# Optimization experiments

Measured on AMD Instinct MI355X. Metric: run time of the kernel, lower is better.

The kernel has to match this reference:

```python
import jax, jax.numpy as jnp
import numpy as np

BN_EPS = 1e-5

def _bn(x, gamma, beta):
    # BatchNorm1d in training mode: batch mean, biased variance
    m = jnp.mean(x, axis=0)
    v = jnp.var(x, axis=0)
    return (x - m) * jax.lax.rsqrt(v + BN_EPS) * gamma + beta

def setup_inputs() -> dict:
    key = jax.random.key(0)
    ks = jax.random.split(key, 12)
    N, E, D, ED = 50000, 600000, 128, 16
    s = lambda k, sh: jax.random.normal(k, sh, dtype=jnp.float32) * 0.05
    return {
        'h': jax.random.normal(ks[0], (N, D), dtype=jnp.float32),
        'edge_index': jax.random.randint(ks[1], (2, E), 0, N, dtype=jnp.int64),
        'edge_attr': jax.random.normal(ks[2], (E, ED), dtype=jnp.float32),
        'ee_w1': s(ks[3], (ED, D)), 'ee_b1': jnp.zeros((D,), jnp.float32),
        'ee_g1': jnp.ones((D,), jnp.float32), 'ee_bb1': jnp.zeros((D,), jnp.float32),
        'ee_w2': s(ks[4], (D, D)), 'ee_b2': jnp.zeros((D,), jnp.float32),
        'mlp_w1': s(ks[5], (D, D)), 'mlp_b1': jnp.zeros((D,), jnp.float32),
        'mlp_g1': jnp.ones((D,), jnp.float32), 'mlp_bb1': jnp.zeros((D,), jnp.float32),
        'mlp_w2': s(ks[6], (D, D)), 'mlp_b2': jnp.zeros((D,), jnp.float32),
        'mlp_g2': jnp.ones((D,), jnp.float32), 'mlp_bb2': jnp.zeros((D,), jnp.float32),
    }

def reference(h, edge_index, edge_attr, ee_w1, ee_b1, ee_g1, ee_bb1, ee_w2, ee_b2,
              mlp_w1, mlp_b1, mlp_g1, mlp_bb1, mlp_w2, mlp_b2, mlp_g2, mlp_bb2):
    N = h.shape[0]
    src, dst = edge_index[0], edge_index[1]
    # edge_encoder: Linear -> BN -> ReLU -> Linear
    e = jax.nn.relu(_bn(edge_attr @ ee_w1 + ee_b1, ee_g1, ee_bb1)) @ ee_w2 + ee_b2  # [E, D]
    # scatter-add edge embeddings to destination nodes
    agg_edge = jax.ops.segment_sum(e, dst, num_segments=N)  # [N, D]
    h = h + agg_edge
    # GINConv (eps=0): mlp(h + sum_{j->i} h_j)
    neigh = jax.ops.segment_sum(h[src], dst, num_segments=N)  # [N, D]
    z = h + neigh
    z = jax.nn.relu(_bn(z @ mlp_w1 + mlp_b1, mlp_g1, mlp_bb1))
    z = jax.nn.relu(_bn(z @ mlp_w2 + mlp_b2, mlp_g2, mlp_bb2))
    return z
```

## Files before the change

kernel.cpp:

```cpp
#include <hip/hip_runtime.h>
#include <hip/hip_bf16.h>

#define DD 128
#define EDIM 16

typedef short v8s __attribute__((ext_vector_type(8)));
typedef float v4f __attribute__((ext_vector_type(4)));

__device__ __forceinline__ float ldf(const void* p, int i, int bf){
  return bf ? __bfloat162float(((const __hip_bfloat16*)p)[i])
            : ((const float*)p)[i];
}
__device__ __forceinline__ float bfu_lo(unsigned u){
  unsigned b = (u & 0xffffu) << 16; float f; __builtin_memcpy(&f,&b,4); return f;
}
__device__ __forceinline__ float bfu_hi(unsigned u){
  unsigned b = u & 0xffff0000u; float f; __builtin_memcpy(&f,&b,4); return f;
}
__device__ __forceinline__ unsigned short f2bf(float f){
  unsigned u; __builtin_memcpy(&u,&f,4);
  unsigned r = (u + 0x7fffu + ((u>>16)&1u)) >> 16;
  return (unsigned short)r;
}
__device__ __forceinline__ unsigned packbf(float a, float b){
  return (unsigned)f2bf(a) | ((unsigned)f2bf(b) << 16);
}

__device__ __forceinline__ void load_attr_row(const void* __restrict__ attr,
                                              int e, int bf, float* a){
  if (bf){
    const uint4* ap = reinterpret_cast<const uint4*>(
        (const __hip_bfloat16*)attr + (size_t)e*EDIM);
    uint4 u0 = ap[0], u1 = ap[1];
    a[0]=bfu_lo(u0.x);  a[1]=bfu_hi(u0.x);  a[2]=bfu_lo(u0.y);  a[3]=bfu_hi(u0.y);
    a[4]=bfu_lo(u0.z);  a[5]=bfu_hi(u0.z);  a[6]=bfu_lo(u0.w);  a[7]=bfu_hi(u0.w);
    a[8]=bfu_lo(u1.x);  a[9]=bfu_hi(u1.x);  a[10]=bfu_lo(u1.y); a[11]=bfu_hi(u1.y);
    a[12]=bfu_lo(u1.z); a[13]=bfu_hi(u1.z); a[14]=bfu_lo(u1.w); a[15]=bfu_hi(u1.w);
  } else {
    const float4* ap = reinterpret_cast<const float4*>(
        (const float*)attr + (size_t)e*EDIM);
    float4 v0=ap[0], v1=ap[1], v2=ap[2], v3=ap[3];
    a[0]=v0.x; a[1]=v0.y; a[2]=v0.z; a[3]=v0.w;
    a[4]=v1.x; a[5]=v1.y; a[6]=v1.z; a[7]=v1.w;
    a[8]=v2.x; a[9]=v2.y; a[10]=v2.z; a[11]=v2.w;
    a[12]=v3.x;a[13]=v3.y;a[14]=v3.z; a[15]=v3.w;
  }
}

__global__ void k_detect(const void* g1, const int* ei, int E, int* flags){
  __shared__ int nz;
  if (threadIdx.x==0) nz = 0;
  __syncthreads();
  long long total = 2LL*E;
  long long stride = (total/1024) & ~1LL;
  if (stride < 2) stride = 2;
  long long idx = (long long)threadIdx.x*stride + 1;
  if (idx < total && ei[idx] != 0) atomicAdd(&nz, 1);
  __syncthreads();
  if (threadIdx.x==0){
    unsigned w = *(const unsigned*)g1;
    flags[0] = (w == 0x3F803F80u) ? 1 : 0;
    flags[1] = (nz == 0) ? 1 : 0;
  }
}

__global__ void k_transB(const void* w0, const void* w1, const void* w2,
                         const void* we1, const int* __restrict__ flags,
                         short* __restrict__ Bt){
  const int bf = flags[0];
  for (int idx = blockIdx.x*blockDim.x + threadIdx.x; idx < 3*16384 + 2048;
       idx += gridDim.x*blockDim.x){
    if (idx < 3*16384){
      int m = idx >> 14, r = idx & 16383;
      int nn = r >> 7, k = r & 127;
      const void* w = (m==0) ? w0 : ((m==1) ? w1 : w2);
      Bt[idx] = (short)f2bf(ldf(w, k*DD + nn, bf));
    } else {
      int r = idx - 3*16384;
      int nn = r >> 4, k = r & 15;
      Bt[idx] = (short)f2bf(ldf(we1, k*DD + nn, bf));
    }
  }
}

__global__ __launch_bounds__(256) void k_attr_moments(
    const void* __restrict__ attr, int E, const int* __restrict__ flags,
    float* __restrict__ Ssum, float* __restrict__ csum)
{
  const int bf = flags[0];
  float acc[136];
  #pragma unroll
  for (int i=0;i<136;++i) acc[i]=0.f;
  float cs[EDIM];
  #pragma unroll
  for (int i=0;i<EDIM;++i) cs[i]=0.f;

  for (int e = blockIdx.x*blockDim.x + threadIdx.x; e < E;
       e += gridDim.x*blockDim.x){
    float a[EDIM];
    load_attr_row(attr, e, bf, a);
    int idx = 0;
    #pragma unroll
    for (int p=0;p<EDIM;++p){
      cs[p] += a[p];
      #pragma unroll
      for (int q=p;q<EDIM;++q){
        acc[idx] = fmaf(a[p], a[q], acc[idx]);
        ++idx;
      }
    }
  }
  #pragma unroll
  for (int i=0;i<136;++i){
    float v = acc[i];
    #pragma unroll
    for (int off=32; off>0; off>>=1) v += __shfl_down(v, off, 64);
    acc[i] = v;
  }
  #pragma unroll
  for (int i=0;i<EDIM;++i){
    float v = cs[i];
    #pragma unroll
    for (int off=32; off>0; off>>=1) v += __shfl_down(v, off, 64);
    cs[i] = v;
  }
  __shared__ float red[4][152];
  const int wave = threadIdx.x >> 6, lane = threadIdx.x & 63;
  if (lane==0){
    for (int i=0;i<136;++i) red[wave][i] = acc[i];
    for (int i=0;i<EDIM;++i) red[wave][136+i] = cs[i];
  }
  __syncthreads();
  const int t = threadIdx.x;
  if (t < 152){
    float s = red[0][t]+red[1][t]+red[2][t]+red[3][t];
    if (t < 136) atomicAdd(&Ssum[t], s);
    else         atomicAdd(&csum[t-136], s);
  }
}

__global__ void k_edge_bn(const void* __restrict__ w1, const void* __restrict__ g,
                          const void* __restrict__ bb,
                          const float* __restrict__ Ssum, const float* __restrict__ csum,
                          float Einv, const int* __restrict__ flags,
                          float* __restrict__ sc, float* __restrict__ sh){
  const int j = threadIdx.x;
  const int bf = flags[0];
  float w[EDIM];
  #pragma unroll
  for (int p=0;p<EDIM;++p) w[p] = ldf(w1, p*DD + j, bf);
  float mu0 = 0.f;
  #pragma unroll
  for (int p=0;p<EDIM;++p) mu0 += csum[p]*Einv*w[p];
  float s2 = 0.f;
  #pragma unroll
  for (int p=0;p<EDIM;++p){
    float acc = 0.f;
    #pragma unroll
    for (int q=0;q<EDIM;++q){
      int tp = p < q ? p : q, tq = p < q ? q : p;
      int idx = 16*tp - (tp*(tp+1))/2 + tq;
      acc += Ssum[idx]*w[q];
    }
    s2 += w[p]*acc;
  }
  float var = s2*Einv - mu0*mu0;
  float scv = ldf(g, j, bf) * rsqrtf(var + 1e-5f);
  sc[j] = scv;
  sh[j] = ldf(bb, j, bf) - mu0*scv;
}

__global__ void k_hist(const int* __restrict__ ei, int E,
                       const int* __restrict__ flags, int* __restrict__ deg){
  const int i64 = flags[1];
  const int2* ei2 = (const int2*)ei;
  for (int e = blockIdx.x*blockDim.x + threadIdx.x; e < E;
       e += gridDim.x*blockDim.x){
    int d = i64 ? ei2[E + e].x : ei[E + e];
    atomicAdd(&deg[d], 1);
  }
}

__global__ void k_scan_partial(const int* __restrict__ deg, int n,
                               int* __restrict__ bsum){
  __shared__ int red[256];
  const int t = threadIdx.x;
  const int base = blockIdx.x*1024;
  int s = 0;
  for (int i = t; i < 1024; i += 256){
    int g = base + i;
    s += (g < n) ? deg[g] : 0;
  }
  red[t] = s; __syncthreads();
  for (int off=128; off>0; off>>=1){
    if (t < off) red[t] += red[t+off];
    __syncthreads();
  }
  if (t==0) bsum[blockIdx.x] = red[0];
}

__global__ void k_scan_tops(int* __restrict__ bsum, int nb, int* __restrict__ total){
  __shared__ int buf[256];
  const int t = threadIdx.x;
  int v = (t < nb) ? bsum[t] : 0;
  buf[t] = v; __syncthreads();
  for (int off=1; off<256; off<<=1){
    int x = (t>=off) ? buf[t-off] : 0;
    __syncthreads();
    buf[t] += x; __syncthreads();
  }
  if (t < nb) bsum[t] = buf[t] - v;
  if (t == 255) *total = buf[255];
}

__global__ void k_scan_final(const int* __restrict__ deg, int n,
                             const int* __restrict__ bsum, const int* __restrict__ total,
                             int* __restrict__ offsets, int* __restrict__ cursor){
  __shared__ int red[256];
  const int t = threadIdx.x;
  const int base = blockIdx.x*1024 + t*4;
  int v[4]; int s = 0;
  #pragma unroll
  for (int k=0;k<4;++k){
    int g = base + k;
    v[k] = (g < n) ? deg[g] : 0;
    s += v[k];
  }
  red[t] = s; __syncthreads();
  for (int off=1; off<256; off<<=1){
    int x = (t>=off) ? red[t-off] : 0;
    __syncthreads();
    red[t] += x; __syncthreads();
  }
  int ex = bsum[blockIdx.x] + red[t] - s;
  #pragma unroll
  for (int k=0;k<4;++k){
    int g = base + k;
    if (g < n){ offsets[g] = ex; cursor[g] = ex; }
    ex += v[k];
  }
  if (blockIdx.x==0 && t==0) offsets[n] = *total;
}

__global__ void k_scatter(const int* __restrict__ ei, const void* __restrict__ attr,
                          int E, const int* __restrict__ flags,
                          int* __restrict__ cursor,
                          int* __restrict__ esrc, unsigned* __restrict__ attrpH){
  const int i64 = flags[1];
  const int bf = flags[0];
  const int2* ei2 = (const int2*)ei;
  for (int e = blockIdx.x*blockDim.x + threadIdx.x; e < E;
       e += gridDim.x*blockDim.x){
    int d = i64 ? ei2[E + e].x : ei[E + e];
    int s = i64 ? ei2[e].x     : ei[e];
    int pp = atomicAdd(&cursor[d], 1);
    esrc[pp] = s;
    float a[EDIM];
    load_attr_row(attr, e, bf, a);
    uint4* dst = reinterpret_cast<uint4*>(attrpH + (size_t)pp*8);
    uint4 o0, o1;
    o0.x = packbf(a[0],a[1]);   o0.y = packbf(a[2],a[3]);
    o0.z = packbf(a[4],a[5]);   o0.w = packbf(a[6],a[7]);
    o1.x = packbf(a[8],a[9]);   o1.y = packbf(a[10],a[11]);
    o1.z = packbf(a[12],a[13]); o1.w = packbf(a[14],a[15]);
    dst[0] = o0; dst[1] = o1;
  }
}

__global__ __launch_bounds__(256) void k_edgemm(
    const short* __restrict__ attrpH, const short* __restrict__ w1t,
    const float* __restrict__ sc, const float* __restrict__ sh,
    int E, __hip_bfloat16* __restrict__ X)
{
  const int t = threadIdx.x;
  const int wv = t >> 6, lane = t & 63, l15 = lane & 15, quad = lane >> 4;
  const int S0 = blockIdx.x*64 + wv*16;
  v8s a = (v8s){0,0,0,0,0,0,0,0};
  if (quad < 2){
    int slot = S0 + l15;
    if (slot < E)
      a = *reinterpret_cast<const v8s*>(&attrpH[(size_t)slot*EDIM + quad*8]);
  }
  v4f acc[8];
  #pragma unroll
  for (int cg=0;cg<8;++cg) acc[cg] = (v4f){0.f,0.f,0.f,0.f};
  #pragma unroll
  for (int cg=0;cg<8;++cg){
    v8s b = (v8s){0,0,0,0,0,0,0,0};
    if (quad < 2)
      b = *reinterpret_cast<const v8s*>(&w1t[(cg*16+l15)*EDIM + quad*8]);
    acc[cg] = __builtin_amdgcn_mfma_f32_16x16x32_bf16(a, b, acc[cg], 0,0,0);
  }
  float scv[8], shv[8];
  #pragma unroll
  for (int cg=0;cg<8;++cg){ scv[cg]=sc[cg*16+l15]; shv[cg]=sh[cg*16+l15]; }
  #pragma unroll
  for (int reg=0;reg<4;++reg){
    int slot = S0 + quad*4 + reg;
    if (slot < E){
      #pragma unroll
      for (int cg=0;cg<8;++cg){
        float x = fmaxf(fmaf(acc[cg][reg], scv[cg], shv[cg]), 0.f);
        X[(size_t)slot*DD + cg*16 + l15] = __float2bfloat16(x);
      }
    }
  }
}

__global__ __launch_bounds__(256) void k_psum(
    const uint4* __restrict__ X16, const int* __restrict__ offsets,
    int n, uint4* __restrict__ PaggH16)
{
  const int wv = threadIdx.x >> 6, lane = threadIdx.x & 63;
  const int g = lane >> 4, c16 = lane & 15;
  for (int i = blockIdx.x*4 + wv; i < n; i += gridDim.x*4){
    const int beg = offsets[i], end = offsets[i+1];
    float a0=0.f,a1=0.f,a2=0.f,a3=0.f,a4=0.f,a5=0.f,a6=0.f,a7=0.f;
    for (int c0 = beg; c0 < end; c0 += 4){
      int r = c0 + g;
      if (r < end){
        uint4 u = X16[(size_t)r*16 + c16];
        a0 += bfu_lo(u.x); a1 += bfu_hi(u.x);
        a2 += bfu_lo(u.y); a3 += bfu_hi(u.y);
        a4 += bfu_lo(u.z); a5 += bfu_hi(u.z);
        a6 += bfu_lo(u.w); a7 += bfu_hi(u.w);
      }
    }
    a0 += __shfl_xor(a0,16,64); a1 += __shfl_xor(a1,16,64);
    a2 += __shfl_xor(a2,16,64); a3 += __shfl_xor(a3,16,64);
    a4 += __shfl_xor(a4,16,64); a5 += __shfl_xor(a5,16,64);
    a6 += __shfl_xor(a6,16,64); a7 += __shfl_xor(a7,16,64);
    a0 += __shfl_xor(a0,32,64); a1 += __shfl_xor(a1,32,64);
    a2 += __shfl_xor(a2,32,64); a3 += __shfl_xor(a3,32,64);
    a4 += __shfl_xor(a4,32,64); a5 += __shfl_xor(a5,32,64);
    a6 += __shfl_xor(a6,32,64); a7 += __shfl_xor(a7,32,64);
    if (lane < 16){
      uint4 o;
      o.x = packbf(a0,a1); o.y = packbf(a2,a3);
      o.z = packbf(a4,a5); o.w = packbf(a6,a7);
      PaggH16[(size_t)i*16 + lane] = o;
    }
  }
}

__global__ __launch_bounds__(256) void k_gather_z(
    const uint4* __restrict__ hnew16, const int* __restrict__ offsets,
    const int* __restrict__ esrc, int n, uint4* __restrict__ zH16)
{
  const int wv = threadIdx.x >> 6, lane = threadIdx.x & 63;
  const int g = lane >> 4, c16 = lane & 15;
  for (int i = blockIdx.x*4 + wv; i < n; i += gridDim.x*4){
    const int beg = offsets[i], end = offsets[i+1];
    float a0=0.f,a1=0.f,a2=0.f,a3=0.f,a4=0.f,a5=0.f,a6=0.f,a7=0.f;
    int c0 = beg;
    for (; c0 + 8 <= end; c0 += 8){
      int s1 = esrc[c0 + g];
      int s2 = esrc[c0 + 4 + g];
      uint4 u = hnew16[(size_t)s1*16 + c16];
      uint4 v = hnew16[(size_t)s2*16 + c16];
      a0 += bfu_lo(u.x)+bfu_lo(v.x); a1 += bfu_hi(u.x)+bfu_hi(v.x);
      a2 += bfu_lo(u.y)+bfu_lo(v.y); a3 += bfu_hi(u.y)+bfu_hi(v.y);
      a4 += bfu_lo(u.z)+bfu_lo(v.z); a5 += bfu_hi(u.z)+bfu_hi(v.z);
      a6 += bfu_lo(u.w)+bfu_lo(v.w); a7 += bfu_hi(u.w)+bfu_hi(v.w);
    }
    for (; c0 < end; c0 += 4){
      int r = c0 + g;
      if (r < end){
        uint4 u = hnew16[(size_t)esrc[r]*16 + c16];
        a0 += bfu_lo(u.x); a1 += bfu_hi(u.x);
        a2 += bfu_lo(u.y); a3 += bfu_hi(u.y);
        a4 += bfu_lo(u.z); a5 += bfu_hi(u.z);
        a6 += bfu_lo(u.w); a7 += bfu_hi(u.w);
      }
    }
    a0 += __shfl_xor(a0,16,64); a1 += __shfl_xor(a1,16,64);
    a2 += __shfl_xor(a2,16,64); a3 += __shfl_xor(a3,16,64);
    a4 += __shfl_xor(a4,16,64); a5 += __shfl_xor(a5,16,64);
    a6 += __shfl_xor(a6,16,64); a7 += __shfl_xor(a7,16,64);
    a0 += __shfl_xor(a0,32,64); a1 += __shfl_xor(a1,32,64);
    a2 += __shfl_xor(a2,32,64); a3 += __shfl_xor(a3,32,64);
    a4 += __shfl_xor(a4,32,64); a5 += __shfl_xor(a5,32,64);
    a6 += __shfl_xor(a6,32,64); a7 += __shfl_xor(a7,32,64);
    if (lane < 16){
      uint4 m = hnew16[(size_t)i*16 + lane];
      uint4 o;
      o.x = packbf(a0+bfu_lo(m.x), a1+bfu_hi(m.x));
      o.y = packbf(a2+bfu_lo(m.y), a3+bfu_hi(m.y));
      o.z = packbf(a4+bfu_lo(m.z), a5+bfu_hi(m.z));
      o.w = packbf(a6+bfu_lo(m.w), a7+bfu_hi(m.w));
      zH16[(size_t)i*16 + lane] = o;
    }
  }
}

__global__ __launch_bounds__(256) void k_gemm_mfma(
    const short* __restrict__ A, const short* __restrict__ Bt,
    const void* __restrict__ bias,
    const float* __restrict__ psc, const float* __restrict__ psh,
    const int* __restrict__ deg, const void* __restrict__ H,
    const int* __restrict__ flags, int n,
    __hip_bfloat16* __restrict__ out, float* __restrict__ stats, int mode)
{
  __shared__ float sb[256];
  const int t = threadIdx.x;
  const int bfi = flags[0];
  sb[t] = 0.f;
  __syncthreads();
  const int wv = t >> 6, lane = t & 63, l15 = lane & 15, quad = lane >> 4;
  const int R0 = blockIdx.x*64 + wv*16;

  v8s a[4];
  {
    const int arow = R0 + l15;
    const bool ok = (arow < n);
    #pragma unroll
    for (int ks=0;ks<4;++ks){
      const int k0 = ks*32 + quad*8;
      uint4 u = {0u,0u,0u,0u};
      if (ok) u = *reinterpret_cast<const uint4*>(&A[(size_t)arow*DD + k0]);
      if (psc){
        float f[8];
        f[0]=bfu_lo(u.x); f[1]=bfu_hi(u.x); f[2]=bfu_lo(u.y); f[3]=bfu_hi(u.y);
        f[4]=bfu_lo(u.z); f[5]=bfu_hi(u.z); f[6]=bfu_lo(u.w); f[7]=bfu_hi(u.w);
        v8s av;
        #pragma unroll
        for (int j=0;j<8;++j)
          av[j] = (short)f2bf(fmaxf(fmaf(f[j], psc[k0+j], psh[k0+j]), 0.f));
        a[ks] = av;
      } else {
        a[ks] = *reinterpret_cast<v8s*>(&u);
      }
    }
  }

  v4f acc[8];
  #pragma unroll
  for (int cg=0;cg<8;++cg) acc[cg] = (v4f){0.f,0.f,0.f,0.f};
  #pragma unroll
  for (int ks=0;ks<4;++ks){
    #pragma unroll
    for (int cg=0;cg<8;++cg){
      v8s b = *reinterpret_cast<const v8s*>(
                &Bt[(cg*16+l15)*DD + ks*32 + quad*8]);
      acc[cg] = __builtin_amdgcn_mfma_f32_16x16x32_bf16(a[ks], b, acc[cg], 0,0,0);
    }
  }

  float bc[8];
  #pragma unroll
  for (int cg=0;cg<8;++cg) bc[cg] = ldf(bias, cg*16 + l15, bfi);
  float ss[8], sq[8];
  #pragma unroll
  for (int cg=0;cg<8;++cg){ ss[cg]=0.f; sq[cg]=0.f; }

  #pragma unroll
  for (int reg=0;reg<4;++reg){
    const int row = R0 + quad*4 + reg;
    if (row < n){
      float degf = (mode==1) ? (float)deg[row] : 0.f;
      #pragma unroll
      for (int cg=0;cg<8;++cg){
        const int col = cg*16 + l15;
        float x = acc[cg][reg];
        if (mode==1) x = fmaf(degf, bc[cg], x) + ldf(H, (size_t)row*DD + col, bfi);
        else         x += bc[cg];
        out[(size_t)row*DD + col] = __float2bfloat16(x);
        ss[cg] += x; sq[cg] += x*x;
      }
    }
  }

  if (stats){
    #pragma unroll
    for (int cg=0;cg<8;++cg){
      float s = ss[cg], q = sq[cg];
      s += __shfl_xor(s, 16, 64); s += __shfl_xor(s, 32, 64);
      q += __shfl_xor(q, 16, 64); q += __shfl_xor(q, 32, 64);
      if (quad == 0){
        atomicAdd(&sb[cg*16 + l15], s);
        atomicAdd(&sb[128 + cg*16 + l15], q);
      }
    }
    __syncthreads();
    atomicAdd(&stats[t], sb[t]);
  }
}

__global__ void k_bn_params(const float* __restrict__ stats, const void* __restrict__ g,
                            const void* __restrict__ bb, const int* __restrict__ flags,
                            float inv_n, float* __restrict__ sc, float* __restrict__ sh){
  const int j = threadIdx.x;
  const int bf = flags[0];
  float mean = stats[j]*inv_n;
  float var  = stats[DD+j]*inv_n - mean*mean;
  float s = ldf(g, j, bf) * rsqrtf(var + 1e-5f);
  sc[j] = s;
  sh[j] = ldf(bb, j, bf) - mean*s;
}

__global__ void k_final(const unsigned* __restrict__ yH,
                        const float* __restrict__ sc, const float* __restrict__ sh,
                        int n, const int* __restrict__ flags, void* __restrict__ out){
  const int bf = flags[0];
  const int nw = n*64;
  for (int i = blockIdx.x*blockDim.x + threadIdx.x; i < nw;
       i += gridDim.x*blockDim.x){
    const int j0 = (i & 63)*2;
    unsigned u = yH[i];
    float v0 = fmaxf(fmaf(bfu_lo(u), sc[j0],   sh[j0]),   0.f);
    float v1 = fmaxf(fmaf(bfu_hi(u), sc[j0+1], sh[j0+1]), 0.f);
    if (bf){
      ((unsigned*)out)[i] = packbf(v0, v1);
    } else {
      *reinterpret_cast<float2*>((float*)out + 2*(size_t)i) = make_float2(v0, v1);
    }
  }
}

extern "C" void kernel_launch(void* const* d_in, const int* in_sizes, int n_in,
                              void* d_out, int out_size, void* d_ws, size_t ws_size,
                              hipStream_t stream)
{
  const void* h       = d_in[0];
  const int*  ei      = (const int*)d_in[1];
  const void* attr    = d_in[2];
  const void* ee_w1   = d_in[3];
  const void* ee_g1   = d_in[5];
  const void* ee_bb1  = d_in[6];
  const void* ee_w2   = d_in[7];
  const void* ee_b2   = d_in[8];
  const void* mlp_w1  = d_in[9];
  const void* mlp_b1  = d_in[10];
  const void* mlp_g1  = d_in[11];
  const void* mlp_bb1 = d_in[12];
  const void* mlp_w2  = d_in[13];
  const void* mlp_b2  = d_in[14];
  const void* mlp_g2  = d_in[15];
  const void* mlp_bb2 = d_in[16];

  const int N = in_sizes[0] / DD;
  const int E = in_sizes[1] / 2;
  const int nb = (N + 1023) / 1024;

  char* p = (char*)d_ws;
  auto alloc = [&](size_t bytes)->char*{
    char* r = p;
    p += (bytes + 255) & ~size_t(255);
    return r;
  };
  int* flags = (int*)alloc(8);
  char* zbase = p;
  int*   deg    = (int*)  zbase;
  float* csum   = (float*)(zbase + (size_t)N*4);
  float* Ssum   = (float*)(zbase + (size_t)N*4 + 64);
  float* stats1 = (float*)(zbase + (size_t)N*4 + 64 + 576);
  float* stats2 = (float*)(zbase + (size_t)N*4 + 64 + 576 + 1024);
  size_t zlen   = (size_t)N*4 + 64 + 576 + 1024 + 1024;
  p += (zlen + 255) & ~size_t(255);
  int*   bsum    = (int*)  alloc(256*4);
  int*   total   = (int*)  alloc(64);
  int*   offsets = (int*)  alloc((size_t)(N+1)*4);
  int*   cursor  = (int*)  alloc((size_t)N*4);
  int*   esrc    = (int*)  alloc((size_t)E*4);
  unsigned* attrpH = (unsigned*)alloc((size_t)E*EDIM*2);
  short* Bt      = (short*)alloc((size_t)(3*DD*DD + DD*EDIM)*2);
  short* w1t     = Bt + 3*DD*DD;
  float* ebn_sc  = (float*)alloc(512);
  float* ebn_sh  = (float*)alloc(512);
  float* sc1     = (float*)alloc(512);
  float* sh1     = (float*)alloc(512);
  float* sc2     = (float*)alloc(512);
  float* sh2     = (float*)alloc(512);
  short* PaggH   = (short*)alloc((size_t)N*DD*2);
  char*  Xreg    = alloc((size_t)E*DD*2);
  __hip_bfloat16* X = (__hip_bfloat16*)Xreg;
  short* hnewH = (short*)Xreg;
  short* zH    = (short*)(Xreg + (size_t)N*DD*2);
  short* y1H   = (short*)(Xreg + (size_t)N*DD*4);
  short* y2H   = (short*)(Xreg + (size_t)N*DD*6);
  (void)ws_size; (void)n_in; (void)out_size;

  const int g64  = (N + 63) / 64;
  const int e64  = (E + 63) / 64;
  const int gseg = (N + 15) / 16;

  hipMemsetAsync(zbase, 0, zlen, stream);
  k_detect<<<1, 1024, 0, stream>>>(ee_g1, ei, E, flags);
  k_transB<<<208, 256, 0, stream>>>(ee_w2, mlp_w1, mlp_w2, ee_w1, flags, Bt);
  k_attr_moments<<<512, 256, 0, stream>>>(attr, E, flags, Ssum, csum);
  k_edge_bn<<<1, 128, 0, stream>>>(ee_w1, ee_g1, ee_bb1, Ssum, csum,
                                   1.0f/(float)E, flags, ebn_sc, ebn_sh);
  k_hist<<<1024, 256, 0, stream>>>(ei, E, flags, deg);
  k_scan_partial<<<nb, 256, 0, stream>>>(deg, N, bsum);
  k_scan_tops<<<1, 256, 0, stream>>>(bsum, nb, total);
  k_scan_final<<<nb, 256, 0, stream>>>(deg, N, bsum, total, offsets, cursor);
  k_scatter<<<1024, 256, 0, stream>>>(ei, attr, E, flags, cursor, esrc, attrpH);

  k_edgemm<<<e64, 256, 0, stream>>>((const short*)attrpH, w1t, ebn_sc, ebn_sh,
                                    E, X);
  k_psum<<<gseg, 256, 0, stream>>>((const uint4*)X, offsets, N, (uint4*)PaggH);

  k_gemm_mfma<<<g64, 256, 0, stream>>>(PaggH, Bt, ee_b2, nullptr, nullptr,
                                       deg, h, flags, N,
                                       (__hip_bfloat16*)hnewH, nullptr, 1);
  k_gather_z<<<gseg, 256, 0, stream>>>((const uint4*)hnewH, offsets, esrc, N,
                                       (uint4*)zH);
  k_gemm_mfma<<<g64, 256, 0, stream>>>(zH, Bt + 16384, mlp_b1, nullptr, nullptr,
                                       nullptr, nullptr, flags, N,
                                       (__hip_bfloat16*)y1H, stats1, 0);
  k_bn_params<<<1, 128, 0, stream>>>(stats1, mlp_g1, mlp_bb1, flags,
                                     1.0f/(float)N, sc1, sh1);
  k_gemm_mfma<<<g64, 256, 0, stream>>>(y1H, Bt + 32768, mlp_b2, sc1, sh1,
                                       nullptr, nullptr, flags, N,
                                       (__hip_bfloat16*)y2H, stats2, 0);
  k_bn_params<<<1, 128, 0, stream>>>(stats2, mlp_g2, mlp_bb2, flags,
                                     1.0f/(float)N, sc2, sh2);

  k_final<<<2048, 256, 0, stream>>>((const unsigned*)y2H, sc2, sh2,
                                    N, flags, d_out);
}
```

Baseline: 472.7 us.

## Fuse edge encoder GEMM with segmented atomic aggregation; MFMA attribute moments

The edge-encoder first layer is now fused with the per-destination reduction. Each wave computes 16 dst-sorted edges and does segmented reductions, then atomically adds partial sums into an fp32 node buffer. This removes the E x 128 bf16 intermediate write and its re-read in the old psum kernel, at the cost of a zeroed N x 128 fp32 buffer, an extra snode array, and float atomics. The attribute second-moment kernel now builds a full 16x16 Gram matrix with one MFMA per 32-edge chunk instead of 136 per-thread scalar FMAs, and the downstream GEMM gains an fp32 input path.

```diff
diff --git a/kernel.cpp b/kernel.cpp
--- a/kernel.cpp
+++ b/kernel.cpp
@@ -85,57 +85,68 @@
 
 __global__ __launch_bounds__(256) void k_attr_moments(
     const void* __restrict__ attr, int E, const int* __restrict__ flags,
-    float* __restrict__ Ssum, float* __restrict__ csum)
+    float* __restrict__ Ssum , float* __restrict__ csum )
 {
+  __shared__ short Ws[4*512];
+  __shared__ float sred[4][256];
+  __shared__ float credu[4][16];
+  const int t = threadIdx.x;
+  const int wv = t >> 6, lane = t & 63, l15 = lane & 15, quad = lane >> 4;
   const int bf = flags[0];
-  float acc[136];
-  #pragma unroll
-  for (int i=0;i<136;++i) acc[i]=0.f;
-  float cs[EDIM];
-  #pragma unroll
-  for (int i=0;i<EDIM;++i) cs[i]=0.f;
-
-  for (int e = blockIdx.x*blockDim.x + threadIdx.x; e < E;
-       e += gridDim.x*blockDim.x){
-    float a[EDIM];
-    load_attr_row(attr, e, bf, a);
-    int idx = 0;
-    #pragma unroll
-    for (int p=0;p<EDIM;++p){
-      cs[p] += a[p];
-      #pragma unroll
-      for (int q=p;q<EDIM;++q){
-        acc[idx] = fmaf(a[p], a[q], acc[idx]);
-        ++idx;
-      }
-    }
-  }
-  #pragma unroll
-  for (int i=0;i<136;++i){
-    float v = acc[i];
-    #pragma unroll
-    for (int off=32; off>0; off>>=1) v += __shfl_down(v, off, 64);
-    acc[i] = v;
-  }
-  #pragma unroll
-  for (int i=0;i<EDIM;++i){
-    float v = cs[i];
-    #pragma unroll
-    for (int off=32; off>0; off>>=1) v += __shfl_down(v, off, 64);
-    cs[i] = v;
-  }
-  __shared__ float red[4][152];
-  const int wave = threadIdx.x >> 6, lane = threadIdx.x & 63;
-  if (lane==0){
-    for (int i=0;i<136;++i) red[wave][i] = acc[i];
-    for (int i=0;i<EDIM;++i) red[wave][136+i] = cs[i];
+  const int el = lane >> 1, half = lane & 1;
+  short* W = &Ws[wv*512];
+
+  v4f acc = (v4f){0.f,0.f,0.f,0.f};
+  float cs[8];
+  #pragma unroll
+  for (int j=0;j<8;++j) cs[j]=0.f;
+
+  const int nchunks = (E + 31) >> 5;
+  for (int c = blockIdx.x*4 + wv; c < nchunks; c += gridDim.x*4){
+    const int e = c*32 + el;
+    const bool ok = (e < E);
+    float f[8];
+    if (bf){
+      uint4 u = {0u,0u,0u,0u};
+      if (ok) u = reinterpret_cast<const uint4*>(attr)[(size_t)e*2 + half];
+      f[0]=bfu_lo(u.x); f[1]=bfu_hi(u.x); f[2]=bfu_lo(u.y); f[3]=bfu_hi(u.y);
+      f[4]=bfu_lo(u.z); f[5]=bfu_hi(u.z); f[6]=bfu_lo(u.w); f[7]=bfu_hi(u.w);
+    } else {
+      float4 v0 = {0,0,0,0}, v1 = {0,0,0,0};
+      if (ok){
+        const float4* ap = reinterpret_cast<const float4*>(attr) +
+                           (size_t)e*4 + half*2;
+        v0 = ap[0]; v1 = ap[1];
+      }
+      f[0]=v0.x; f[1]=v0.y; f[2]=v0.z; f[3]=v0.w;
+      f[4]=v1.x; f[5]=v1.y; f[6]=v1.z; f[7]=v1.w;
+    }
+    #pragma unroll
+    for (int j=0;j<8;++j){
+      cs[j] += f[j];
+      W[(half*8 + j)*32 + el] = (short)f2bf(f[j]);
+    }
+    v8s a = *reinterpret_cast<const v8s*>(&W[l15*32 + quad*8]);
+    acc = __builtin_amdgcn_mfma_f32_16x16x32_bf16(a, a, acc, 0,0,0);
+  }
+
+  #pragma unroll
+  for (int r=0;r<4;++r) sred[wv][(quad*4 + r)*16 + l15] = acc[r];
+  #pragma unroll
+  for (int j=0;j<8;++j){
+    #pragma unroll
+    for (int off=2; off<64; off<<=1) cs[j] += __shfl_xor(cs[j], off, 64);
+  }
+  if (lane < 2){
+    #pragma unroll
+    for (int j=0;j<8;++j) credu[wv][lane*8 + j] = cs[j];
   }
   __syncthreads();
-  const int t = threadIdx.x;
-  if (t < 152){
-    float s = red[0][t]+red[1][t]+red[2][t]+red[3][t];
-    if (t < 136) atomicAdd(&Ssum[t], s);
-    else         atomicAdd(&csum[t-136], s);
+  float s = sred[0][t]+sred[1][t]+sred[2][t]+sred[3][t];
+  atomicAdd(&Ssum[t], s);
+  if (t < 16){
+    float s2 = credu[0][t]+credu[1][t]+credu[2][t]+credu[3][t];
+    atomicAdd(&csum[t], s2);
   }
 }
 
@@ -157,11 +168,7 @@
   for (int p=0;p<EDIM;++p){
     float acc = 0.f;
     #pragma unroll
-    for (int q=0;q<EDIM;++q){
-      int tp = p < q ? p : q, tq = p < q ? q : p;
-      int idx = 16*tp - (tp*(tp+1))/2 + tq;
-      acc += Ssum[idx]*w[q];
-    }
+    for (int q=0;q<EDIM;++q) acc += Ssum[p*16 + q]*w[q];
     s2 += w[p]*acc;
   }
   float var = s2*Einv - mu0*mu0;
@@ -244,8 +251,8 @@
 
 __global__ void k_scatter(const int* __restrict__ ei, const void* __restrict__ attr,
                           int E, const int* __restrict__ flags,
-                          int* __restrict__ cursor,
-                          int* __restrict__ esrc, unsigned* __restrict__ attrpH){
+                          int* __restrict__ cursor, int* __restrict__ esrc,
+                          int* __restrict__ snode, unsigned* __restrict__ attrpH){
   const int i64 = flags[1];
   const int bf = flags[0];
   const int2* ei2 = (const int2*)ei;
@@ -255,6 +262,7 @@
     int s = i64 ? ei2[e].x     : ei[e];
     int pp = atomicAdd(&cursor[d], 1);
     esrc[pp] = s;
+    snode[pp] = d;
     float a[EDIM];
     load_attr_row(attr, e, bf, a);
     uint4* dst = reinterpret_cast<uint4*>(attrpH + (size_t)pp*8);
@@ -267,79 +275,68 @@
   }
 }
 
-__global__ __launch_bounds__(256) void k_edgemm(
+__global__ __launch_bounds__(256) void k_edgeagg(
     const short* __restrict__ attrpH, const short* __restrict__ w1t,
     const float* __restrict__ sc, const float* __restrict__ sh,
-    int E, __hip_bfloat16* __restrict__ X)
+    const int* __restrict__ offsets, const int* __restrict__ snode,
+    int n, int E, float* __restrict__ Pagg)
 {
   const int t = threadIdx.x;
   const int wv = t >> 6, lane = t & 63, l15 = lane & 15, quad = lane >> 4;
-  const int S0 = blockIdx.x*64 + wv*16;
+  const int W0 = blockIdx.x*64 + wv*16;
+  if (W0 >= E) return;
+
   v8s a = (v8s){0,0,0,0,0,0,0,0};
   if (quad < 2){
-    int slot = S0 + l15;
+    int slot = W0 + l15;
     if (slot < E)
       a = *reinterpret_cast<const v8s*>(&attrpH[(size_t)slot*EDIM + quad*8]);
   }
-  v4f acc[8];
-  #pragma unroll
-  for (int cg=0;cg<8;++cg) acc[cg] = (v4f){0.f,0.f,0.f,0.f};
+  float val[8][4];
   #pragma unroll
   for (int cg=0;cg<8;++cg){
     v8s b = (v8s){0,0,0,0,0,0,0,0};
     if (quad < 2)
       b = *reinterpret_cast<const v8s*>(&w1t[(cg*16+l15)*EDIM + quad*8]);
-    acc[cg] = __builtin_amdgcn_mfma_f32_16x16x32_bf16(a, b, acc[cg], 0,0,0);
-  }
-  float scv[8], shv[8];
-  #pragma unroll
-  for (int cg=0;cg<8;++cg){ scv[cg]=sc[cg*16+l15]; shv[cg]=sh[cg*16+l15]; }
-  #pragma unroll
-  for (int reg=0;reg<4;++reg){
-    int slot = S0 + quad*4 + reg;
-    if (slot < E){
+    v4f acc = (v4f){0.f,0.f,0.f,0.f};
+    acc = __builtin_amdgcn_mfma_f32_16x16x32_bf16(a, b, acc, 0,0,0);
+    const float scv = sc[cg*16+l15], shv = sh[cg*16+l15];
+    #pragma unroll
+    for (int reg=0;reg<4;++reg)
+      val[cg][reg] = fmaxf(fmaf(acc[reg], scv, shv), 0.f);
+  }
+
+  int i = snode[W0];
+  const int Wend = (W0 + 16 < E) ? (W0 + 16) : E;
+  int segb = W0;
+  while (segb < Wend && i < n){
+    int oe = offsets[i+1];
+    int sege = (oe < Wend) ? oe : Wend;
+    if (sege > segb){
+      float part[8];
+      #pragma unroll
+      for (int cg=0;cg<8;++cg) part[cg] = 0.f;
+      #pragma unroll
+      for (int reg=0;reg<4;++reg){
+        int s = W0 + quad*4 + reg;
+        if (s >= segb && s < sege){
+          #pragma unroll
+          for (int cg=0;cg<8;++cg) part[cg] += val[cg][reg];
+        }
+      }
       #pragma unroll
       for (int cg=0;cg<8;++cg){
-        float x = fmaxf(fmaf(acc[cg][reg], scv[cg], shv[cg]), 0.f);
-        X[(size_t)slot*DD + cg*16 + l15] = __float2bfloat16(x);
-      }
-    }
-  }
-}
-
-__global__ __launch_bounds__(256) void k_psum(
-    const uint4* __restrict__ X16, const int* __restrict__ offsets,
-    int n, uint4* __restrict__ PaggH16)
-{
-  const int wv = threadIdx.x >> 6, lane = threadIdx.x & 63;
-  const int g = lane >> 4, c16 = lane & 15;
-  for (int i = blockIdx.x*4 + wv; i < n; i += gridDim.x*4){
-    const int beg = offsets[i], end = offsets[i+1];
-    float a0=0.f,a1=0.f,a2=0.f,a3=0.f,a4=0.f,a5=0.f,a6=0.f,a7=0.f;
-    for (int c0 = beg; c0 < end; c0 += 4){
-      int r = c0 + g;
-      if (r < end){
-        uint4 u = X16[(size_t)r*16 + c16];
-        a0 += bfu_lo(u.x); a1 += bfu_hi(u.x);
-        a2 += bfu_lo(u.y); a3 += bfu_hi(u.y);
-        a4 += bfu_lo(u.z); a5 += bfu_hi(u.z);
-        a6 += bfu_lo(u.w); a7 += bfu_hi(u.w);
-      }
-    }
-    a0 += __shfl_xor(a0,16,64); a1 += __shfl_xor(a1,16,64);
-    a2 += __shfl_xor(a2,16,64); a3 += __shfl_xor(a3,16,64);
-    a4 += __shfl_xor(a4,16,64); a5 += __shfl_xor(a5,16,64);
-    a6 += __shfl_xor(a6,16,64); a7 += __shfl_xor(a7,16,64);
-    a0 += __shfl_xor(a0,32,64); a1 += __shfl_xor(a1,32,64);
-    a2 += __shfl_xor(a2,32,64); a3 += __shfl_xor(a3,32,64);
-    a4 += __shfl_xor(a4,32,64); a5 += __shfl_xor(a5,32,64);
-    a6 += __shfl_xor(a6,32,64); a7 += __shfl_xor(a7,32,64);
-    if (lane < 16){
-      uint4 o;
-      o.x = packbf(a0,a1); o.y = packbf(a2,a3);
-      o.z = packbf(a4,a5); o.w = packbf(a6,a7);
-      PaggH16[(size_t)i*16 + lane] = o;
-    }
+        part[cg] += __shfl_xor(part[cg], 16, 64);
+        part[cg] += __shfl_xor(part[cg], 32, 64);
+      }
+      if (quad == 0){
+        #pragma unroll
+        for (int cg=0;cg<8;++cg)
+          atomicAdd(&Pagg[(size_t)i*DD + cg*16 + l15], part[cg]);
+      }
+      segb = sege;
+    }
+    ++i;
   }
 }
 
@@ -394,8 +391,8 @@
 }
 
 __global__ __launch_bounds__(256) void k_gemm_mfma(
-    const short* __restrict__ A, const short* __restrict__ Bt,
-    const void* __restrict__ bias,
+    const short* __restrict__ A, const float* __restrict__ Af32,
+    const short* __restrict__ Bt, const void* __restrict__ bias,
     const float* __restrict__ psc, const float* __restrict__ psh,
     const int* __restrict__ deg, const void* __restrict__ H,
     const int* __restrict__ flags, int n,
@@ -416,19 +413,34 @@
     #pragma unroll
     for (int ks=0;ks<4;++ks){
       const int k0 = ks*32 + quad*8;
-      uint4 u = {0u,0u,0u,0u};
-      if (ok) u = *reinterpret_cast<const uint4*>(&A[(size_t)arow*DD + k0]);
-      if (psc){
-        float f[8];
-        f[0]=bfu_lo(u.x); f[1]=bfu_hi(u.x); f[2]=bfu_lo(u.y); f[3]=bfu_hi(u.y);
-        f[4]=bfu_lo(u.z); f[5]=bfu_hi(u.z); f[6]=bfu_lo(u.w); f[7]=bfu_hi(u.w);
+      float f[8];
+      if (Af32){
+        float4 v0 = {0,0,0,0}, v1 = {0,0,0,0};
+        if (ok){
+          const float4* ap = reinterpret_cast<const float4*>(
+              Af32 + (size_t)arow*DD + k0);
+          v0 = ap[0]; v1 = ap[1];
+        }
+        f[0]=v0.x; f[1]=v0.y; f[2]=v0.z; f[3]=v0.w;
+        f[4]=v1.x; f[5]=v1.y; f[6]=v1.z; f[7]=v1.w;
         v8s av;
         #pragma unroll
-        for (int j=0;j<8;++j)
-          av[j] = (short)f2bf(fmaxf(fmaf(f[j], psc[k0+j], psh[k0+j]), 0.f));
+        for (int j=0;j<8;++j) av[j] = (short)f2bf(f[j]);
         a[ks] = av;
       } else {
-        a[ks] = *reinterpret_cast<v8s*>(&u);
+        uint4 u = {0u,0u,0u,0u};
+        if (ok) u = *reinterpret_cast<const uint4*>(&A[(size_t)arow*DD + k0]);
+        if (psc){
+          f[0]=bfu_lo(u.x); f[1]=bfu_hi(u.x); f[2]=bfu_lo(u.y); f[3]=bfu_hi(u.y);
+          f[4]=bfu_lo(u.z); f[5]=bfu_hi(u.z); f[6]=bfu_lo(u.w); f[7]=bfu_hi(u.w);
+          v8s av;
+          #pragma unroll
+          for (int j=0;j<8;++j)
+            av[j] = (short)f2bf(fmaxf(fmaf(f[j], psc[k0+j], psh[k0+j]), 0.f));
+          a[ks] = av;
+        } else {
+          a[ks] = *reinterpret_cast<v8s*>(&u);
+        }
       }
     }
   }
@@ -553,15 +565,17 @@
   int*   deg    = (int*)  zbase;
   float* csum   = (float*)(zbase + (size_t)N*4);
   float* Ssum   = (float*)(zbase + (size_t)N*4 + 64);
-  float* stats1 = (float*)(zbase + (size_t)N*4 + 64 + 576);
-  float* stats2 = (float*)(zbase + (size_t)N*4 + 64 + 576 + 1024);
-  size_t zlen   = (size_t)N*4 + 64 + 576 + 1024 + 1024;
+  float* stats1 = (float*)(zbase + (size_t)N*4 + 64 + 1024);
+  float* stats2 = (float*)(zbase + (size_t)N*4 + 64 + 2048);
+  float* Pagg   = (float*)(zbase + (size_t)N*4 + 64 + 3072);
+  size_t zlen   = (size_t)N*4 + 64 + 3072 + (size_t)N*DD*4;
   p += (zlen + 255) & ~size_t(255);
   int*   bsum    = (int*)  alloc(256*4);
   int*   total   = (int*)  alloc(64);
   int*   offsets = (int*)  alloc((size_t)(N+1)*4);
   int*   cursor  = (int*)  alloc((size_t)N*4);
   int*   esrc    = (int*)  alloc((size_t)E*4);
+  int*   snode   = (int*)  alloc((size_t)E*4);
   unsigned* attrpH = (unsigned*)alloc((size_t)E*EDIM*2);
   short* Bt      = (short*)alloc((size_t)(3*DD*DD + DD*EDIM)*2);
   short* w1t     = Bt + 3*DD*DD;
@@ -571,13 +585,10 @@
   float* sh1     = (float*)alloc(512);
   float* sc2     = (float*)alloc(512);
   float* sh2     = (float*)alloc(512);
-  short* PaggH   = (short*)alloc((size_t)N*DD*2);
-  char*  Xreg    = alloc((size_t)E*DD*2);
-  __hip_bfloat16* X = (__hip_bfloat16*)Xreg;
-  short* hnewH = (short*)Xreg;
-  short* zH    = (short*)(Xreg + (size_t)N*DD*2);
-  short* y1H   = (short*)(Xreg + (size_t)N*DD*4);
-  short* y2H   = (short*)(Xreg + (size_t)N*DD*6);
+  short* hnewH   = (short*)alloc((size_t)N*DD*2);
+  short* zH      = (short*)alloc((size_t)N*DD*2);
+  short* y1H     = (short*)alloc((size_t)N*DD*2);
+  short* y2H     = (short*)alloc((size_t)N*DD*2);
   (void)ws_size; (void)n_in; (void)out_size;
 
   const int g64  = (N + 63) / 64;
@@ -587,32 +598,32 @@
   hipMemsetAsync(zbase, 0, zlen, stream);
   k_detect<<<1, 1024, 0, stream>>>(ee_g1, ei, E, flags);
   k_transB<<<208, 256, 0, stream>>>(ee_w2, mlp_w1, mlp_w2, ee_w1, flags, Bt);
-  k_attr_moments<<<512, 256, 0, stream>>>(attr, E, flags, Ssum, csum);
+  k_attr_moments<<<256, 256, 0, stream>>>(attr, E, flags, Ssum, csum);
   k_edge_bn<<<1, 128, 0, stream>>>(ee_w1, ee_g1, ee_bb1, Ssum, csum,
                                    1.0f/(float)E, flags, ebn_sc, ebn_sh);
   k_hist<<<1024, 256, 0, stream>>>(ei, E, flags, deg);
   k_scan_partial<<<nb, 256, 0, stream>>>(deg, N, bsum);
   k_scan_tops<<<1, 256, 0, stream>>>(bsum, nb, total);
   k_scan_final<<<nb, 256, 0, stream>>>(deg, N, bsum, total, offsets, cursor);
-  k_scatter<<<1024, 256, 0, stream>>>(ei, attr, E, flags, cursor, esrc, attrpH);
-
-  k_edgemm<<<e64, 256, 0, stream>>>((const short*)attrpH, w1t, ebn_sc, ebn_sh,
-                                    E, X);
-  k_psum<<<gseg, 256, 0, stream>>>((const uint4*)X, offsets, N, (uint4*)PaggH);
-
-  k_gemm_mfma<<<g64, 256, 0, stream>>>(PaggH, Bt, ee_b2, nullptr, nullptr,
-                                       deg, h, flags, N,
+  k_scatter<<<1024, 256, 0, stream>>>(ei, attr, E, flags, cursor, esrc,
+                                      snode, attrpH);
+
+  k_edgeagg<<<e64, 256, 0, stream>>>((const short*)attrpH, w1t, ebn_sc, ebn_sh,
+                                     offsets, snode, N, E, Pagg);
+
+  k_gemm_mfma<<<g64, 256, 0, stream>>>(nullptr, Pagg, Bt, ee_b2,
+                                       nullptr, nullptr, deg, h, flags, N,
                                        (__hip_bfloat16*)hnewH, nullptr, 1);
   k_gather_z<<<gseg, 256, 0, stream>>>((const uint4*)hnewH, offsets, esrc, N,
                                        (uint4*)zH);
-  k_gemm_mfma<<<g64, 256, 0, stream>>>(zH, Bt + 16384, mlp_b1, nullptr, nullptr,
-                                       nullptr, nullptr, flags, N,
-                                       (__hip_bfloat16*)y1H, stats1, 0);
+  k_gemm_mfma<<<g64, 256, 0, stream>>>(zH, nullptr, Bt + 16384, mlp_b1,
+                                       nullptr, nullptr, nullptr, nullptr,
+                                       flags, N, (__hip_bfloat16*)y1H, stats1, 0);
   k_bn_params<<<1, 128, 0, stream>>>(stats1, mlp_g1, mlp_bb1, flags,
                                      1.0f/(float)N, sc1, sh1);
-  k_gemm_mfma<<<g64, 256, 0, stream>>>(y1H, Bt + 32768, mlp_b2, sc1, sh1,
-                                       nullptr, nullptr, flags, N,
-                                       (__hip_bfloat16*)y2H, stats2, 0);
+  k_gemm_mfma<<<g64, 256, 0, stream>>>(y1H, nullptr, Bt + 32768, mlp_b2,
+                                       sc1, sh1, nullptr, nullptr,
+                                       flags, N, (__hip_bfloat16*)y2H, stats2, 0);
   k_bn_params<<<1, 128, 0, stream>>>(stats2, mlp_g2, mlp_bb2, flags,
                                      1.0f/(float)N, sc2, sh2);
 
```

Result: faster. 444.5 us (-6.0%).
